# Performance work log

Hardware: AMD Instinct MI355X
Metric: run time of the kernel (lower is better)

The kernel has to match this reference:

```python
import jax, jax.numpy as jnp
import numpy as np

N = 50000      # nodes
E = 320000     # edges
D_NODE = 256   # node feature size
D_EDGE = 128   # raw edge feature size
T_DIM = 64     # time encoder out_channels
H = 8          # heads (auto_num_heads(256) -> 8)
C = 32         # per-head dim = 256 // 8
D_E_IN = D_EDGE + T_DIM  # edge_dim into lin_edge


def setup_inputs() -> dict:
    key = jax.random.key(0)
    ks = jax.random.split(key, 16)
    s_n = 1.0 / np.sqrt(D_NODE)
    s_e = 1.0 / np.sqrt(D_E_IN)
    return {
        "edge_tuples": jax.random.randint(ks[0], (2, E), 0, N, dtype=jnp.int64)
        if jax.config.jax_enable_x64 else jax.random.randint(ks[0], (2, E), 0, N),
        "edge_feats": jax.random.normal(ks[1], (E, D_EDGE), jnp.float32),
        "edge_times_rel": jax.random.uniform(ks[2], (E,), jnp.float32) * 100.0,
        "node_feats": jax.random.normal(ks[3], (N, D_NODE), jnp.float32),
        # time encoder: Linear(1, T_DIM) followed by cos
        "w_time": jax.random.normal(ks[4], (T_DIM,), jnp.float32),
        "b_time": jax.random.normal(ks[5], (T_DIM,), jnp.float32),
        # TransformerConv linears (out = H*C = 256)
        "Wq": jax.random.normal(ks[6], (H * C, D_NODE), jnp.float32) * s_n,
        "bq": jnp.zeros((H * C,), jnp.float32),
        "Wk": jax.random.normal(ks[7], (H * C, D_NODE), jnp.float32) * s_n,
        "bk": jnp.zeros((H * C,), jnp.float32),
        "Wv": jax.random.normal(ks[8], (H * C, D_NODE), jnp.float32) * s_n,
        "bv": jnp.zeros((H * C,), jnp.float32),
        "We": jax.random.normal(ks[9], (H * C, D_E_IN), jnp.float32) * s_e,  # lin_edge, no bias
        "Ws": jax.random.normal(ks[10], (H * C, D_NODE), jnp.float32) * s_n,  # lin_skip
        "bs": jnp.zeros((H * C,), jnp.float32),
    }


def reference(edge_tuples, edge_feats, edge_times_rel, node_feats,
              w_time, b_time, Wq, bq, Wk, bk, Wv, bv, We, Ws, bs):
    n_nodes = node_feats.shape[0]
    n_edges = edge_tuples.shape[1]
    src, dst = edge_tuples[0], edge_tuples[1]

    # TGN time encoder: cos(t * w + b)  -> [E, T_DIM]
    tfeat = jnp.cos(edge_times_rel[:, None] * w_time[None, :] + b_time)
    e_attr = jnp.concatenate([tfeat, edge_feats], axis=1)  # [E, T_DIM + D_EDGE]

    # dense per-node projections, then gather per edge
    q = (node_feats @ Wq.T + bq)[dst].reshape(n_edges, H, C)
    k = (node_feats @ Wk.T + bk)[src].reshape(n_edges, H, C)
    v = (node_feats @ Wv.T + bv)[src].reshape(n_edges, H, C)
    ep = (e_attr @ We.T).reshape(n_edges, H, C)

    k = k + ep
    alpha = jnp.sum(q * k, axis=-1) / jnp.sqrt(jnp.asarray(C, q.dtype))  # [E, H]

    # segment softmax over edges grouped by destination node
    m = jax.ops.segment_max(alpha, dst, num_segments=n_nodes)  # [N, H]
    m = jnp.where(jnp.isfinite(m), m, 0.0)
    ea = jnp.exp(alpha - m[dst])
    denom = jax.ops.segment_sum(ea, dst, num_segments=n_nodes)
    a = ea / (denom[dst] + 1e-16)  # [E, H]

    # weighted scatter-aggregate of (value + edge) messages
    msg = a[:, :, None] * (v + ep)  # [E, H, C]
    out = jax.ops.segment_sum(msg, dst, num_segments=n_nodes).reshape(n_nodes, H * C)

    # root / skip connection
    out = out + node_feats @ Ws.T + bs
    return out
```

## Files before the change

kernel.cpp:

```cpp
#include <hip/hip_runtime.h>
#include <hip/hip_bf16.h>
#include <math.h>

#define NN 50000
#define NE 320000
#define SCAN_NBLK ((NN + 255) / 256)

typedef __attribute__((ext_vector_type(8))) short bf16x8;
typedef __attribute__((ext_vector_type(4))) float floatx4;

static __device__ __forceinline__ unsigned pack2bf(float a, float b) {
    __hip_bfloat162 h = __float22bfloat162_rn(make_float2(a, b));
    return *reinterpret_cast<unsigned*>(&h);
}
static __device__ __forceinline__ unsigned short f2bf(float x) {
    __hip_bfloat16 h = __float2bfloat16(x);
    return *reinterpret_cast<unsigned short*>(&h);
}
static __device__ __forceinline__ float bf2f(unsigned short u) {
    return __uint_as_float(((unsigned)u) << 16);
}
static __device__ __forceinline__ void gload_lds16(const void* g, void* l) {
    __builtin_amdgcn_global_load_lds(
        (const __attribute__((address_space(1))) void*)g,
        (__attribute__((address_space(3))) void*)l, 16, 0, 0);
}

__global__ __launch_bounds__(256)
void cvt_bf16_kernel(const float* __restrict__ in,
                     unsigned short* __restrict__ out, int n8)
{
    int t = blockIdx.x * 256 + threadIdx.x;
    if (t >= n8) return;
    const float4* p = (const float4*)in + (size_t)t * 2;
    float4 a = p[0], b = p[1];
    uint4 u;
    u.x = pack2bf(a.x, a.y); u.y = pack2bf(a.z, a.w);
    u.z = pack2bf(b.x, b.y); u.w = pack2bf(b.z, b.w);
    ((uint4*)out)[t] = u;
}

__global__ __launch_bounds__(256)
void tf_kernel(const float* __restrict__ tvals,
               const float* __restrict__ w_time,
               const float* __restrict__ b_time,
               unsigned short* __restrict__ eab)
{
    int t = blockIdx.x * 256 + threadIdx.x;
    int e = t >> 3, part = t & 7;
    if (e >= NE) return;
    float tv = tvals[e];
    int k = part * 8;
    float v[8];
    #pragma unroll
    for (int i = 0; i < 8; ++i)
        v[i] = cosf(fmaf(tv, w_time[k + i], b_time[k + i]));
    uint4 u;
    u.x = pack2bf(v[0], v[1]); u.y = pack2bf(v[2], v[3]);
    u.z = pack2bf(v[4], v[5]); u.w = pack2bf(v[6], v[7]);
    *(uint4*)(eab + (size_t)e * 192 + k) = u;
}

__global__ __launch_bounds__(256)
void efcvt_kernel(const float* __restrict__ efeat,
                  unsigned short* __restrict__ eab)
{
    int t = blockIdx.x * 256 + threadIdx.x;
    int e = t >> 4, part = t & 15;
    if (e >= NE) return;
    const float4* p = (const float4*)(efeat + (size_t)e * 128 + part * 8);
    float4 a = p[0], b = p[1];
    uint4 u;
    u.x = pack2bf(a.x, a.y); u.y = pack2bf(a.z, a.w);
    u.z = pack2bf(b.x, b.y); u.w = pack2bf(b.z, b.w);
    *(uint4*)(eab + (size_t)e * 192 + 64 + part * 8) = u;
}

__global__ __launch_bounds__(256)
void node_gemm_kernel(const unsigned short* __restrict__ Xb,
                      const unsigned short* __restrict__ Wqb,
                      const unsigned short* __restrict__ Wkb,
                      const unsigned short* __restrict__ Wvb,
                      const unsigned short* __restrict__ Wsb,
                      const float* __restrict__ bq, const float* __restrict__ bk,
                      const float* __restrict__ bv, const float* __restrict__ bs,
                      unsigned short* __restrict__ qb,
                      unsigned short* __restrict__ kb,
                      unsigned short* __restrict__ vb,
                      float* __restrict__ outS)
{
    const int m0  = blockIdx.x * 128;
    const int ct  = blockIdx.y;
    const int mat = ct >> 1, half = ct & 1;
    const int colbase = half * 128;

    const unsigned short* __restrict__ W;
    const float* __restrict__ bias;
    switch (mat) {
        case 0:  W = Wqb; bias = bq; break;
        case 1:  W = Wkb; bias = bk; break;
        case 2:  W = Wvb; bias = bv; break;
        default: W = Wsb; bias = bs; break;
    }
    W += (size_t)colbase * 256;

    __shared__ __align__(16) unsigned char smem[32768];
    short* sA = (short*)smem;
    short* sB = (short*)(smem + 16384);

    const int tid  = threadIdx.x;
    const int lane = tid & 63;
    const int wave = tid >> 6;
    const int wm   = (wave & 1) * 64;
    const int wn   = (wave >> 1) * 64;
    const int lr   = lane & 15;
    const int lq   = lane >> 4;

    const int srow = tid >> 3;
    const int scol = (tid & 7) * 8;

    floatx4 acc[4][4];
    #pragma unroll
    for (int i = 0; i < 4; ++i)
        #pragma unroll
        for (int j = 0; j < 4; ++j)
            acc[i][j] = (floatx4){0.f, 0.f, 0.f, 0.f};

    for (int k0 = 0; k0 < 256; k0 += 64) {
        #pragma unroll
        for (int p = 0; p < 4; ++p) {
            int arow = m0 + p * 32 + srow;
            if (arow > NN - 1) arow = NN - 1;
            gload_lds16(Xb + (size_t)arow * 256 + k0 + scol,
                        (char*)sA + p * 4096 + wave * 1024);
            gload_lds16(W + (size_t)(p * 32 + srow) * 256 + k0 + scol,
                        (char*)sB + p * 4096 + wave * 1024);
        }
        __syncthreads();

        #pragma unroll
        for (int ks = 0; ks < 2; ++ks) {
            bf16x8 af[4], bfr[4];
            #pragma unroll
            for (int i = 0; i < 4; ++i)
                af[i] = *(const bf16x8*)&sA[(wm + i * 16 + lr) * 64 + ks * 32 + lq * 8];
            #pragma unroll
            for (int j = 0; j < 4; ++j)
                bfr[j] = *(const bf16x8*)&sB[(wn + j * 16 + lr) * 64 + ks * 32 + lq * 8];
            #pragma unroll
            for (int i = 0; i < 4; ++i)
                #pragma unroll
                for (int j = 0; j < 4; ++j)
                    acc[i][j] = __builtin_amdgcn_mfma_f32_16x16x32_bf16(
                        af[i], bfr[j], acc[i][j], 0, 0, 0);
        }
        __syncthreads();
    }

    if (mat < 3) {
        unsigned short* __restrict__ Cb = (mat == 0) ? qb : (mat == 1) ? kb : vb;
        unsigned short* sOut = (unsigned short*)smem;
        for (int ch = 0; ch < 4; ++ch) {
            __syncthreads();
            if ((ch >> 1) == (wave & 1)) {
                int ibase = (ch & 1) * 2;
                #pragma unroll
                for (int ii = 0; ii < 2; ++ii) {
                    int i = ibase + ii;
                    #pragma unroll
                    for (int j = 0; j < 4; ++j) {
                        int col = wn + j * 16 + lr;
                        float bb = bias[colbase + col];
                        #pragma unroll
                        for (int r = 0; r < 4; ++r) {
                            int rowc = ii * 16 + lq * 4 + r;
                            sOut[rowc * 136 + col] = f2bf(acc[i][j][r] + bb);
                        }
                    }
                }
            }
            __syncthreads();
            #pragma unroll
            for (int p = 0; p < 2; ++p) {
                int rowc = p * 16 + (tid >> 4);
                int off  = (tid & 15) * 8;
                int grow = m0 + ch * 32 + rowc;
                if (grow < NN) {
                    uint4 u = *(const uint4*)&sOut[rowc * 136 + off];
                    *(uint4*)&Cb[(size_t)grow * 256 + colbase + off] = u;
                }
            }
        }
    } else {
        float* sOutF = (float*)smem;
        for (int ch = 0; ch < 8; ++ch) {
            __syncthreads();
            if ((ch >> 2) == (wave & 1)) {
                int i = ch & 3;
                #pragma unroll
                for (int j = 0; j < 4; ++j) {
                    int col = wn + j * 16 + lr;
                    float bb = bias[colbase + col];
                    #pragma unroll
                    for (int r = 0; r < 4; ++r) {
                        int rowc = lq * 4 + r;
                        sOutF[rowc * 132 + col] = acc[i][j][r] + bb;
                    }
                }
            }
            __syncthreads();
            #pragma unroll
            for (int p = 0; p < 2; ++p) {
                int rowc = p * 8 + (tid >> 5);
                int off  = (tid & 31) * 4;
                int grow = m0 + ch * 16 + rowc;
                if (grow < NN) {
                    float4 f = *(const float4*)&sOutF[rowc * 132 + off];
                    *(float4*)&outS[(size_t)grow * 256 + colbase + off] = f;
                }
            }
        }
    }
}

__global__ __launch_bounds__(256)
void edge_gemm_kernel(const unsigned short* __restrict__ eab,
                      const unsigned short* __restrict__ Web,
                      unsigned short* __restrict__ epb)
{
    const int m0 = blockIdx.x * 128;
    const int n0 = blockIdx.y * 128;

    __shared__ __align__(16) unsigned char smem[32768];
    short* sA = (short*)smem;
    short* sB = (short*)(smem + 16384);

    const int tid  = threadIdx.x;
    const int lane = tid & 63;
    const int wave = tid >> 6;
    const int wm   = (wave & 1) * 64;
    const int wn   = (wave >> 1) * 64;
    const int lr   = lane & 15;
    const int lq   = lane >> 4;

    const int srow = tid >> 3;
    const int scol = (tid & 7) * 8;

    floatx4 acc[4][4];
    #pragma unroll
    for (int i = 0; i < 4; ++i)
        #pragma unroll
        for (int j = 0; j < 4; ++j)
            acc[i][j] = (floatx4){0.f, 0.f, 0.f, 0.f};

    for (int k0 = 0; k0 < 192; k0 += 64) {
        #pragma unroll
        for (int p = 0; p < 4; ++p) {
            gload_lds16(eab + (size_t)(m0 + p * 32 + srow) * 192 + k0 + scol,
                        (char*)sA + p * 4096 + wave * 1024);
            gload_lds16(Web + (size_t)(n0 + p * 32 + srow) * 192 + k0 + scol,
                        (char*)sB + p * 4096 + wave * 1024);
        }
        __syncthreads();

        #pragma unroll
        for (int ks = 0; ks < 2; ++ks) {
            bf16x8 af[4], bfr[4];
            #pragma unroll
            for (int i = 0; i < 4; ++i)
                af[i] = *(const bf16x8*)&sA[(wm + i * 16 + lr) * 64 + ks * 32 + lq * 8];
            #pragma unroll
            for (int j = 0; j < 4; ++j)
                bfr[j] = *(const bf16x8*)&sB[(wn + j * 16 + lr) * 64 + ks * 32 + lq * 8];
            #pragma unroll
            for (int i = 0; i < 4; ++i)
                #pragma unroll
                for (int j = 0; j < 4; ++j)
                    acc[i][j] = __builtin_amdgcn_mfma_f32_16x16x32_bf16(
                        af[i], bfr[j], acc[i][j], 0, 0, 0);
        }
        __syncthreads();
    }

    unsigned short* sOut = (unsigned short*)smem;
    for (int ch = 0; ch < 4; ++ch) {
        __syncthreads();
        if ((ch >> 1) == (wave & 1)) {
            int ibase = (ch & 1) * 2;
            #pragma unroll
            for (int ii = 0; ii < 2; ++ii) {
                int i = ibase + ii;
                #pragma unroll
                for (int j = 0; j < 4; ++j) {
                    int col = wn + j * 16 + lr;
                    #pragma unroll
                    for (int r = 0; r < 4; ++r) {
                        int rowc = ii * 16 + lq * 4 + r;
                        sOut[rowc * 136 + col] = f2bf(acc[i][j][r]);
                    }
                }
            }
        }
        __syncthreads();
        #pragma unroll
        for (int p = 0; p < 2; ++p) {
            int rowc = p * 16 + (tid >> 4);
            int off  = (tid & 15) * 8;
            int grow = m0 + ch * 32 + rowc;
            uint4 u = *(const uint4*)&sOut[rowc * 136 + off];
            *(uint4*)&epb[(size_t)grow * 256 + n0 + off] = u;
        }
    }
}

__global__ __launch_bounds__(256)
void deg_kernel(const int* __restrict__ et, int* __restrict__ deg)
{
    int e = blockIdx.x * 256 + threadIdx.x;
    if (e < NE) atomicAdd(&deg[et[NE + e]], 1);
}

__global__ __launch_bounds__(256)
void blocksum_kernel(const int* __restrict__ deg, int* __restrict__ bsum)
{
    int idx = blockIdx.x * 256 + threadIdx.x;
    int v = (idx < NN) ? deg[idx] : 0;
    #pragma unroll
    for (int off = 1; off < 64; off <<= 1) v += __shfl_xor(v, off);
    __shared__ int s[4];
    if ((threadIdx.x & 63) == 0) s[threadIdx.x >> 6] = v;
    __syncthreads();
    if (threadIdx.x == 0) bsum[blockIdx.x] = s[0] + s[1] + s[2] + s[3];
}

__global__ __launch_bounds__(256)
void bscan_kernel(int* __restrict__ bsum, int* __restrict__ rowstart)
{
    __shared__ int s[256];
    int t = threadIdx.x;
    int v = (t < SCAN_NBLK) ? bsum[t] : 0;
    s[t] = v;
    __syncthreads();
    #pragma unroll
    for (int off = 1; off < 256; off <<= 1) {
        int u = (t >= off) ? s[t - off] : 0;
        __syncthreads();
        s[t] += u;
        __syncthreads();
    }
    if (t < SCAN_NBLK) bsum[t] = (t == 0) ? 0 : s[t - 1];
    if (t == 0) rowstart[NN] = s[SCAN_NBLK - 1];
}

__global__ __launch_bounds__(256)
void chunkscan_kernel(const int* __restrict__ deg, const int* __restrict__ bsum,
                      int* __restrict__ rowstart, int* __restrict__ cursor)
{
    __shared__ int s[256];
    int t = threadIdx.x;
    int idx = blockIdx.x * 256 + t;
    int v = (idx < NN) ? deg[idx] : 0;
    s[t] = v;
    __syncthreads();
    #pragma unroll
    for (int off = 1; off < 256; off <<= 1) {
        int u = (t >= off) ? s[t - off] : 0;
        __syncthreads();
        s[t] += u;
        __syncthreads();
    }
    if (idx < NN) {
        int ex = bsum[blockIdx.x] + s[t] - v;
        rowstart[idx] = ex;
        cursor[idx]   = ex;
    }
}

__global__ __launch_bounds__(256)
void scatter_kernel(const int* __restrict__ et,
                    int* __restrict__ cursor,
                    int* __restrict__ elist, int* __restrict__ slist)
{
    int e = blockIdx.x * 256 + threadIdx.x;
    if (e < NE) {
        int d   = et[NE + e];
        int pos = atomicAdd(&cursor[d], 1);
        elist[pos] = e;
        slist[pos] = et[e];
    }
}

__global__ __launch_bounds__(256)
void fused_agg_kernel(const int* __restrict__ slist,
                      const int* __restrict__ rowstart,
                      const int* __restrict__ elist,
                      const unsigned short* __restrict__ qb,
                      const unsigned short* __restrict__ kb,
                      const unsigned short* __restrict__ vb,
                      const unsigned short* __restrict__ epb,
                      float* __restrict__ out)
{
    const int n = blockIdx.x * 4 + (threadIdx.x >> 6);
    if (n >= NN) return;
    const int lane = threadIdx.x & 63;

    ushort4 qu = *(const ushort4*)(qb + (size_t)n * 256 + lane * 4);
    const float q0 = bf2f(qu.x), q1 = bf2f(qu.y), q2 = bf2f(qu.z), q3 = bf2f(qu.w);

    float acc0 = 0.f, acc1 = 0.f, acc2 = 0.f, acc3 = 0.f, accd = 0.f;

    const int s0 = rowstart[n];
    const int s1 = rowstart[n + 1];

    for (int i = s0; i < s1; ++i) {
        const int e   = elist[i];
        const int src = slist[i];
        ushort4 ku = *(const ushort4*)(kb  + (size_t)src * 256 + lane * 4);
        ushort4 pu = *(const ushort4*)(epb + (size_t)e   * 256 + lane * 4);
        ushort4 vu = *(const ushort4*)(vb  + (size_t)src * 256 + lane * 4);

        float kp0 = bf2f(ku.x) + bf2f(pu.x);
        float kp1 = bf2f(ku.y) + bf2f(pu.y);
        float kp2 = bf2f(ku.z) + bf2f(pu.z);
        float kp3 = bf2f(ku.w) + bf2f(pu.w);

        float part = q0 * kp0 + q1 * kp1 + q2 * kp2 + q3 * kp3;
        part += __shfl_xor(part, 1);
        part += __shfl_xor(part, 2);
        part += __shfl_xor(part, 4);

        float eav = __expf(part * 0.17677669529663687f);
        acc0 = fmaf(eav, bf2f(vu.x) + bf2f(pu.x), acc0);
        acc1 = fmaf(eav, bf2f(vu.y) + bf2f(pu.y), acc1);
        acc2 = fmaf(eav, bf2f(vu.z) + bf2f(pu.z), acc2);
        acc3 = fmaf(eav, bf2f(vu.w) + bf2f(pu.w), acc3);
        accd += eav;
    }

    const float inv = 1.f / (accd + 1e-16f);
    float* po = out + (size_t)n * 256 + lane * 4;
    float4 o = *(const float4*)po;
    o.x = fmaf(acc0, inv, o.x);
    o.y = fmaf(acc1, inv, o.y);
    o.z = fmaf(acc2, inv, o.z);
    o.w = fmaf(acc3, inv, o.w);
    *(float4*)po = o;
}

extern "C" void kernel_launch(void* const* d_in, const int* in_sizes, int n_in,
                              void* d_out, int out_size, void* d_ws, size_t ws_size,
                              hipStream_t stream)
{
    const int*   et  = (const int*)  d_in[0];
    const float* ef  = (const float*)d_in[1];
    const float* tv  = (const float*)d_in[2];
    const float* nf  = (const float*)d_in[3];
    const float* w_t = (const float*)d_in[4];
    const float* b_t = (const float*)d_in[5];
    const float* Wq  = (const float*)d_in[6];
    const float* bq  = (const float*)d_in[7];
    const float* Wk  = (const float*)d_in[8];
    const float* bk  = (const float*)d_in[9];
    const float* Wv  = (const float*)d_in[10];
    const float* bv  = (const float*)d_in[11];
    const float* We  = (const float*)d_in[12];
    const float* Ws  = (const float*)d_in[13];
    const float* bs  = (const float*)d_in[14];
    float* out = (float*)d_out;

    unsigned short* qb  = (unsigned short*)d_ws;
    unsigned short* kb  = qb  + (size_t)NN * 256;
    unsigned short* vb  = kb  + (size_t)NN * 256;
    unsigned short* epb = vb  + (size_t)NN * 256;
    unsigned short* nfb = epb + (size_t)NE * 256;
    unsigned short* eab = nfb + (size_t)NN * 256;
    unsigned short* Wqb = eab + (size_t)NE * 192;
    unsigned short* Wkb = Wqb + 65536;
    unsigned short* Wvb = Wkb + 65536;
    unsigned short* Wsb = Wvb + 65536;
    unsigned short* Web = Wsb + 65536;
    int* deg      = (int*)(Web + 49152);
    int* rowstart = deg + NN;
    int* cursor   = rowstart + NN + 1;
    int* elist    = cursor + NN;
    int* slist    = elist + NE;
    int* bsum     = slist + NE;
    size_t need   = (size_t)((char*)(bsum + SCAN_NBLK) - (char*)d_ws);
    if (ws_size < need) return;

    hipMemsetAsync(deg, 0, (size_t)NN * sizeof(int), stream);

    cvt_bf16_kernel<<<(NN * 256 / 8 + 255) / 256, 256, 0, stream>>>(nf, nfb, NN * 256 / 8);
    cvt_bf16_kernel<<<32, 256, 0, stream>>>(Wq, Wqb, 8192);
    cvt_bf16_kernel<<<32, 256, 0, stream>>>(Wk, Wkb, 8192);
    cvt_bf16_kernel<<<32, 256, 0, stream>>>(Wv, Wvb, 8192);
    cvt_bf16_kernel<<<32, 256, 0, stream>>>(Ws, Wsb, 8192);
    cvt_bf16_kernel<<<24, 256, 0, stream>>>(We, Web, 6144);
    tf_kernel<<<(NE * 8 + 255) / 256, 256, 0, stream>>>(tv, w_t, b_t, eab);
    efcvt_kernel<<<(NE * 16 + 255) / 256, 256, 0, stream>>>(ef, eab);

    node_gemm_kernel<<<dim3((NN + 127) / 128, 8), 256, 0, stream>>>(
        nfb, Wqb, Wkb, Wvb, Wsb, bq, bk, bv, bs, qb, kb, vb, out);

    edge_gemm_kernel<<<dim3(NE / 128, 2), 256, 0, stream>>>(eab, Web, epb);

    deg_kernel<<<(NE + 255) / 256, 256, 0, stream>>>(et, deg);
    blocksum_kernel<<<SCAN_NBLK, 256, 0, stream>>>(deg, bsum);
    bscan_kernel<<<1, 256, 0, stream>>>(bsum, rowstart);
    chunkscan_kernel<<<SCAN_NBLK, 256, 0, stream>>>(deg, bsum, rowstart, cursor);
    scatter_kernel<<<(NE + 255) / 256, 256, 0, stream>>>(et, cursor, elist, slist);

    fused_agg_kernel<<<(NN + 3) / 4, 256, 0, stream>>>(
        slist, rowstart, elist, qb, kb, vb, epb, out);
}
```

Before: 661.3 us.

## Process two edges per wave with half-wave split, 16-byte loads, and interleaved edge list

The aggregation kernel now splits each 64-lane wave into two halves that handle different edges at the same time, with each lane loading 8 bf16 values (16 bytes) instead of 4. The loop is unrolled to four edges per iteration so more memory requests are in flight, and the halves are combined with a cross-half shuffle at the end. Edge id and source are packed into one int2 list to save a load, and edge projection reads use nontemporal loads. This adds tail masking logic and more registers per thread.

```diff
diff --git a/kernel.cpp b/kernel.cpp
--- a/kernel.cpp
+++ b/kernel.cpp
@@ -8,6 +8,7 @@
 
 typedef __attribute__((ext_vector_type(8))) short bf16x8;
 typedef __attribute__((ext_vector_type(4))) float floatx4;
+typedef __attribute__((ext_vector_type(4))) unsigned int uintx4;
 
 static __device__ __forceinline__ unsigned pack2bf(float a, float b) {
     __hip_bfloat162 h = __float22bfloat162_rn(make_float2(a, b));
@@ -19,6 +20,12 @@
 }
 static __device__ __forceinline__ float bf2f(unsigned short u) {
     return __uint_as_float(((unsigned)u) << 16);
+}
+static __device__ __forceinline__ float bflo(unsigned u) {
+    return __uint_as_float(u << 16);
+}
+static __device__ __forceinline__ float bfhi(unsigned u) {
+    return __uint_as_float(u & 0xffff0000u);
 }
 static __device__ __forceinline__ void gload_lds16(const void* g, void* l) {
     __builtin_amdgcn_global_load_lds(
@@ -379,21 +386,53 @@
 __global__ __launch_bounds__(256)
 void scatter_kernel(const int* __restrict__ et,
                     int* __restrict__ cursor,
-                    int* __restrict__ elist, int* __restrict__ slist)
+                    int2* __restrict__ eslist)
 {
     int e = blockIdx.x * 256 + threadIdx.x;
     if (e < NE) {
         int d   = et[NE + e];
         int pos = atomicAdd(&cursor[d], 1);
-        elist[pos] = e;
-        slist[pos] = et[e];
-    }
-}
-
-__global__ __launch_bounds__(256)
-void fused_agg_kernel(const int* __restrict__ slist,
+        eslist[pos] = make_int2(e, et[e]);
+    }
+}
+
+static __device__ __forceinline__ void edge_proc(
+    uint4 ku, uint4 vu, uintx4 eu, const float* q, float mask,
+    float* a, float& accd)
+{
+    float pe0 = bflo(eu[0]), pe1 = bfhi(eu[0]);
+    float pe2 = bflo(eu[1]), pe3 = bfhi(eu[1]);
+    float pe4 = bflo(eu[2]), pe5 = bfhi(eu[2]);
+    float pe6 = bflo(eu[3]), pe7 = bfhi(eu[3]);
+
+    float part;
+    part = q[0] * (bflo(ku.x) + pe0);
+    part = fmaf(q[1], bfhi(ku.x) + pe1, part);
+    part = fmaf(q[2], bflo(ku.y) + pe2, part);
+    part = fmaf(q[3], bfhi(ku.y) + pe3, part);
+    part = fmaf(q[4], bflo(ku.z) + pe4, part);
+    part = fmaf(q[5], bfhi(ku.z) + pe5, part);
+    part = fmaf(q[6], bflo(ku.w) + pe6, part);
+    part = fmaf(q[7], bfhi(ku.w) + pe7, part);
+    part += __shfl_xor(part, 1);
+    part += __shfl_xor(part, 2);
+
+    float ea = __expf(part * 0.17677669529663687f) * mask;
+
+    a[0] = fmaf(ea, bflo(vu.x) + pe0, a[0]);
+    a[1] = fmaf(ea, bfhi(vu.x) + pe1, a[1]);
+    a[2] = fmaf(ea, bflo(vu.y) + pe2, a[2]);
+    a[3] = fmaf(ea, bfhi(vu.y) + pe3, a[3]);
+    a[4] = fmaf(ea, bflo(vu.z) + pe4, a[4]);
+    a[5] = fmaf(ea, bfhi(vu.z) + pe5, a[5]);
+    a[6] = fmaf(ea, bflo(vu.w) + pe6, a[6]);
+    a[7] = fmaf(ea, bfhi(vu.w) + pe7, a[7]);
+    accd += ea;
+}
+
+__global__ __launch_bounds__(256)
+void fused_agg_kernel(const int2* __restrict__ eslist,
                       const int* __restrict__ rowstart,
-                      const int* __restrict__ elist,
                       const unsigned short* __restrict__ qb,
                       const unsigned short* __restrict__ kb,
                       const unsigned short* __restrict__ vb,
@@ -403,48 +442,75 @@
     const int n = blockIdx.x * 4 + (threadIdx.x >> 6);
     if (n >= NN) return;
     const int lane = threadIdx.x & 63;
-
-    ushort4 qu = *(const ushort4*)(qb + (size_t)n * 256 + lane * 4);
-    const float q0 = bf2f(qu.x), q1 = bf2f(qu.y), q2 = bf2f(qu.z), q3 = bf2f(qu.w);
-
-    float acc0 = 0.f, acc1 = 0.f, acc2 = 0.f, acc3 = 0.f, accd = 0.f;
+    const int half = lane >> 5;
+    const int co   = (lane & 31) * 8;
+
+    uint4 qu = *(const uint4*)(qb + (size_t)n * 256 + co);
+    float q[8] = { bflo(qu.x), bfhi(qu.x), bflo(qu.y), bfhi(qu.y),
+                   bflo(qu.z), bfhi(qu.z), bflo(qu.w), bfhi(qu.w) };
+
+    float a[8] = {0.f, 0.f, 0.f, 0.f, 0.f, 0.f, 0.f, 0.f};
+    float accd = 0.f;
 
     const int s0 = rowstart[n];
     const int s1 = rowstart[n + 1];
 
-    for (int i = s0; i < s1; ++i) {
-        const int e   = elist[i];
-        const int src = slist[i];
-        ushort4 ku = *(const ushort4*)(kb  + (size_t)src * 256 + lane * 4);
-        ushort4 pu = *(const ushort4*)(epb + (size_t)e   * 256 + lane * 4);
-        ushort4 vu = *(const ushort4*)(vb  + (size_t)src * 256 + lane * 4);
-
-        float kp0 = bf2f(ku.x) + bf2f(pu.x);
-        float kp1 = bf2f(ku.y) + bf2f(pu.y);
-        float kp2 = bf2f(ku.z) + bf2f(pu.z);
-        float kp3 = bf2f(ku.w) + bf2f(pu.w);
-
-        float part = q0 * kp0 + q1 * kp1 + q2 * kp2 + q3 * kp3;
-        part += __shfl_xor(part, 1);
-        part += __shfl_xor(part, 2);
-        part += __shfl_xor(part, 4);
-
-        float eav = __expf(part * 0.17677669529663687f);
-        acc0 = fmaf(eav, bf2f(vu.x) + bf2f(pu.x), acc0);
-        acc1 = fmaf(eav, bf2f(vu.y) + bf2f(pu.y), acc1);
-        acc2 = fmaf(eav, bf2f(vu.z) + bf2f(pu.z), acc2);
-        acc3 = fmaf(eav, bf2f(vu.w) + bf2f(pu.w), acc3);
-        accd += eav;
-    }
-
-    const float inv = 1.f / (accd + 1e-16f);
-    float* po = out + (size_t)n * 256 + lane * 4;
-    float4 o = *(const float4*)po;
-    o.x = fmaf(acc0, inv, o.x);
-    o.y = fmaf(acc1, inv, o.y);
-    o.z = fmaf(acc2, inv, o.z);
-    o.w = fmaf(acc3, inv, o.w);
-    *(float4*)po = o;
+    int i = s0;
+    for (; i + 4 <= s1; i += 4) {
+        const int2 pA = eslist[i + half];
+        const int2 pB = eslist[i + 2 + half];
+        uint4 kA = *(const uint4*)(kb + (size_t)pA.y * 256 + co);
+        uint4 vA = *(const uint4*)(vb + (size_t)pA.y * 256 + co);
+        uintx4 eA = __builtin_nontemporal_load(
+                        (const uintx4*)(epb + (size_t)pA.x * 256 + co));
+        uint4 kB = *(const uint4*)(kb + (size_t)pB.y * 256 + co);
+        uint4 vB = *(const uint4*)(vb + (size_t)pB.y * 256 + co);
+        uintx4 eB = __builtin_nontemporal_load(
+                        (const uintx4*)(epb + (size_t)pB.x * 256 + co));
+
+        edge_proc(kA, vA, eA, q, 1.f, a, accd);
+        edge_proc(kB, vB, eB, q, 1.f, a, accd);
+    }
+    for (; i + 2 <= s1; i += 2) {
+        const int2 pA = eslist[i + half];
+        uint4 kA = *(const uint4*)(kb + (size_t)pA.y * 256 + co);
+        uint4 vA = *(const uint4*)(vb + (size_t)pA.y * 256 + co);
+        uintx4 eA = __builtin_nontemporal_load(
+                        (const uintx4*)(epb + (size_t)pA.x * 256 + co));
+        edge_proc(kA, vA, eA, q, 1.f, a, accd);
+    }
+    if (i < s1) {
+        int idx = i + half;
+        float mask = (idx < s1) ? 1.f : 0.f;
+        if (idx >= s1) idx = s1 - 1;
+        const int2 pA = eslist[idx];
+        uint4 kA = *(const uint4*)(kb + (size_t)pA.y * 256 + co);
+        uint4 vA = *(const uint4*)(vb + (size_t)pA.y * 256 + co);
+        uintx4 eA = __builtin_nontemporal_load(
+                        (const uintx4*)(epb + (size_t)pA.x * 256 + co));
+        edge_proc(kA, vA, eA, q, mask, a, accd);
+    }
+
+    #pragma unroll
+    for (int j = 0; j < 8; ++j) a[j] += __shfl_xor(a[j], 32);
+    accd += __shfl_xor(accd, 32);
+
+    if (half == 0) {
+        const float inv = 1.f / (accd + 1e-16f);
+        float* po = out + (size_t)n * 256 + co;
+        float4 o0 = ((const float4*)po)[0];
+        float4 o1 = ((const float4*)po)[1];
+        o0.x = fmaf(a[0], inv, o0.x);
+        o0.y = fmaf(a[1], inv, o0.y);
+        o0.z = fmaf(a[2], inv, o0.z);
+        o0.w = fmaf(a[3], inv, o0.w);
+        o1.x = fmaf(a[4], inv, o1.x);
+        o1.y = fmaf(a[5], inv, o1.y);
+        o1.z = fmaf(a[6], inv, o1.z);
+        o1.w = fmaf(a[7], inv, o1.w);
+        ((float4*)po)[0] = o0;
+        ((float4*)po)[1] = o1;
+    }
 }
 
 extern "C" void kernel_launch(void* const* d_in, const int* in_sizes, int n_in,
@@ -482,13 +548,12 @@
     int* deg      = (int*)(Web + 49152);
     int* rowstart = deg + NN;
     int* cursor   = rowstart + NN + 1;
-    int* elist    = cursor + NN;
-    int* slist    = elist + NE;
-    int* bsum     = slist + NE;
+    int2* eslist  = (int2*)(cursor + NN);
+    int* bsum     = (int*)(eslist + NE);
     size_t need   = (size_t)((char*)(bsum + SCAN_NBLK) - (char*)d_ws);
     if (ws_size < need) return;
 
-    hipMemsetAsync(deg, 0, (size_t)NN * sizeof(int), stream);
+    (void)hipMemsetAsync(deg, 0, (size_t)NN * sizeof(int), stream);
 
     cvt_bf16_kernel<<<(NN * 256 / 8 + 255) / 256, 256, 0, stream>>>(nf, nfb, NN * 256 / 8);
     cvt_bf16_kernel<<<32, 256, 0, stream>>>(Wq, Wqb, 8192);
@@ -508,8 +573,8 @@
     blocksum_kernel<<<SCAN_NBLK, 256, 0, stream>>>(deg, bsum);
     bscan_kernel<<<1, 256, 0, stream>>>(bsum, rowstart);
     chunkscan_kernel<<<SCAN_NBLK, 256, 0, stream>>>(deg, bsum, rowstart, cursor);
-    scatter_kernel<<<(NE + 255) / 256, 256, 0, stream>>>(et, cursor, elist, slist);
+    scatter_kernel<<<(NE + 255) / 256, 256, 0, stream>>>(et, cursor, eslist);
 
     fused_agg_kernel<<<(NN + 3) / 4, 256, 0, stream>>>(
-        slist, rowstart, elist, qb, kb, vb, epb, out);
-}
+        eslist, rowstart, qb, kb, vb, epb, out);
+}
```

Result: faster. 640.2 us (-3.2%).
